# Kernel optimization log

Hardware: AMD Instinct MI355X
Metric: run time of the kernel (lower is better)

## Reference

```python
import jax, jax.numpy as jnp
import numpy as np


def _conv1d(x, w, b):
    # x: (B, Cin, T_padded), w: (Cout, Cin, K), b: (Cout,) -> (B, Cout, T_out)
    y = jax.lax.conv_general_dilated(
        x, w, window_strides=(1,), padding='VALID',
        dimension_numbers=('NCH', 'OIH', 'NCH'))
    return y + b[None, :, None]


def setup_inputs() -> dict:
    key = jax.random.key(0)
    ks = jax.random.split(key, 7)
    B, C, T, H = 32, 64, 8192, 256
    W = 0.05  # small init scale (xavier-ish, keeps exp(log_s) stable)
    return {
        'x': jax.random.normal(ks[0], (B, C, T), dtype=jnp.float32),
        'w_in': jax.random.normal(ks[1], (H, C, 3), dtype=jnp.float32) * W,
        'b_in': jax.random.normal(ks[2], (H,), dtype=jnp.float32) * W,
        'w_mid': jax.random.normal(ks[3], (H, H, 3), dtype=jnp.float32) * W,
        'b_mid': jax.random.normal(ks[4], (H,), dtype=jnp.float32) * W,
        'w_out': jax.random.normal(ks[5], (2 * C, H, 3), dtype=jnp.float32) * W,
        'b_out': jax.random.normal(ks[6], (2 * C,), dtype=jnp.float32) * W,
        'alpha': jnp.ones((1, C, 1), dtype=jnp.float32),
        'beta': jnp.zeros((1, C, 1), dtype=jnp.float32),
    }


def reference(x, w_in, b_in, w_mid, b_mid, w_out, b_out, alpha, beta):
    C = x.shape[1]
    # causal shift: drop last timestep, left-pad 3 -> conv(k=3) yields T outputs
    x_in = jnp.pad(x[:, :, :-1], ((0, 0), (0, 0), (3, 0)))
    rs = _conv1d(x_in, w_in, b_in)                                  # (B, H, T)
    rs = _conv1d(jnp.pad(rs, ((0, 0), (0, 0), (2, 0))), w_mid, b_mid)
    rs = _conv1d(jnp.pad(rs, ((0, 0), (0, 0), (2, 0))), w_out, b_out)  # (B, 2C, T)
    log_s, t = rs[:, :C, :], rs[:, C:, :]
    log_s = alpha * jnp.tanh(log_s) + beta
    z = jnp.exp(log_s) * x + t
    return z
```

## Files before the change

kernel.cpp:

```cpp
#include <hip/hip_runtime.h>
#include <cmath>

typedef __attribute__((ext_vector_type(8))) short short8;
typedef __attribute__((ext_vector_type(4))) float f32x4;

#define B_   32
#define C_   64
#define T_   8192
#define H_   256
#define TT   64

#define XS_ROWB 144
#define RS_ROWB 528
#define RS1_OFF 0
#define RS2_OFF 43296
#define XS_OFF  43296
#define RS3_OFF 0
#define LDS_BYTES 78144

#define A1_SZ 98304
#define A2_SZ 393216
#define A3_SZ 196608
#define AW_TOTAL (A1_SZ + A2_SZ + A3_SZ)

__device__ __forceinline__ unsigned short f2bf(float f) {
    unsigned u = __builtin_bit_cast(unsigned, f);
    u += 0x7fffu + ((u >> 16) & 1u);
    return (unsigned short)(u >> 16);
}

__device__ __forceinline__ unsigned cvtpk(float lo, float hi) {
    unsigned r;
    asm("v_cvt_pk_bf16_f32 %0, %1, %2" : "=v"(r) : "v"(lo), "v"(hi));
    return r;
}

__global__ void pack_w(const float* __restrict__ w1, const float* __restrict__ w2,
                       const float* __restrict__ w3, unsigned short* __restrict__ ws)
{
    int id = blockIdx.x * 256 + threadIdx.x;
    const float* w; int MT, KT, Cin; unsigned short* dst;
    if (id < 6144)       {             w = w1; MT = 16; KT = 2; Cin = 64;  dst = ws; }
    else if (id < 30720) { id -= 6144; w = w2; MT = 16; KT = 8; Cin = 256; dst = ws + A1_SZ/2; }
    else if (id < 43008) { id -= 30720; w = w3; MT = 8; KT = 8; Cin = 256; dst = ws + (A1_SZ+A2_SZ)/2; }
    else return;
    const int lane = id & 63;
    int f = id >> 6;
    const int kt = f % KT; f /= KT;
    const int mt = f % MT;
    const int tap = f / MT;
    const int h  = mt*16 + (lane & 15);
    const int c0 = kt*32 + (lane >> 4)*8;
    unsigned short* o = dst + (size_t)id * 8;
    #pragma unroll
    for (int j = 0; j < 8; ++j)
        o[j] = f2bf(w[((size_t)(h*Cin + c0 + j))*3 + tap]);
}

__device__ __forceinline__ short8 ldA(const char* base, int frag, int lane) {
    return *(const short8*)(base + ((size_t)frag*64 + lane)*16);
}

__global__ __launch_bounds__(512, 4)
void arflow_mfma(const float* __restrict__ x,
                 const float* __restrict__ b_in, const float* __restrict__ b_mid,
                 const float* __restrict__ b_out,
                 const float* __restrict__ alpha, const float* __restrict__ beta,
                 const char* __restrict__ wpk,
                 float* __restrict__ out)
{
    __shared__ __align__(16) char lds[LDS_BYTES];
    unsigned short* xs = (unsigned short*)(lds + XS_OFF);
    char* rs1 = lds + RS1_OFF;
    char* rs2 = lds + RS2_OFF;

    const char* wA1 = wpk;
    const char* wA2 = wpk + A1_SZ;
    const char* wA3 = wpk + A1_SZ + A2_SZ;

    const int b   = blockIdx.y;
    const int t0  = blockIdx.x * TT;
    const int tid = threadIdx.x;
    const int lane = tid & 63;
    const int wid  = tid >> 6;
    const int l15 = lane & 15, l4 = lane >> 4;

    {
        const int rr = tid & 63, cg = tid >> 6;
        #pragma unroll
        for (int p = 0; p < 4; ++p) {
            const int c = cg*8 + p*2;
            const float* xc0 = x + ((size_t)b*C_ + c)*T_;
            const float* xc1 = xc0 + T_;
            {
                const int r = rr; const int t = t0 - 19 + r;
                float v0 = 0.f, v1 = 0.f;
                if (t >= 0) { v0 = xc0[t]; v1 = xc1[t]; }
                *(unsigned*)(&xs[r*72 + c]) = cvtpk(v0, v1);
            }
            {
                const int r = rr + 64;
                if (r < 83) {
                    const int t = t0 - 19 + r;
                    *(unsigned*)(&xs[r*72 + c]) = cvtpk(xc0[t], xc1[t]);
                }
            }
        }
        if (tid < 264) ((unsigned*)rs1)[tid] = 0u;
    }
    __syncthreads();

    {
        const int mt0 = wid*2;
        f32x4 acc[2][5];
        #pragma unroll
        for (int m = 0; m < 2; ++m) {
            const f32x4 bv = *(const f32x4*)(b_in + (mt0+m)*16 + l4*4);
            #pragma unroll
            for (int nt = 0; nt < 5; ++nt) acc[m][nt] = bv;
        }
        int nb[5];
        #pragma unroll
        for (int nt = 0; nt < 5; ++nt)
            nb[nt] = XS_OFF + (16*nt + l15)*XS_ROWB + l4*16;
        short8 Ab[2][2];
        #pragma unroll
        for (int m = 0; m < 2; ++m) Ab[0][m] = ldA(wA1, (mt0+m)*2, lane);
        #pragma unroll
        for (int kt = 0; kt < 6; ++kt) {
            const int cur = kt & 1;
            const int tap = kt >> 1, ck = kt & 1;
            if (kt < 5) {
                const int kn = kt+1, tapn = kn>>1, ckn = kn&1;
                #pragma unroll
                for (int m = 0; m < 2; ++m)
                    Ab[cur^1][m] = ldA(wA1, (tapn*16 + mt0+m)*2 + ckn, lane);
            }
            __builtin_amdgcn_s_setprio(1);
            #pragma unroll
            for (int nt = 0; nt < 5; ++nt) {
                const short8 Bf = *(const short8*)(lds + nb[nt] + tap*XS_ROWB + ck*64);
                #pragma unroll
                for (int m = 0; m < 2; ++m)
                    acc[m][nt] = __builtin_amdgcn_mfma_f32_16x16x32_bf16(Ab[cur][m], Bf, acc[m][nt], 0, 0, 0);
            }
            __builtin_amdgcn_s_setprio(0);
        }
        #pragma unroll
        for (int nt = 0; nt < 5; ++nt) {
            const int tt16 = 16*nt + l15;
            const int t = t0 - 16 + tt16;
            char* dst0 = rs1 + (2 + tt16)*RS_ROWB;
            #pragma unroll
            for (int m = 0; m < 2; ++m) {
                const f32x4 a = acc[m][nt];
                unsigned long long pk = 0ull;
                if (t >= 0)
                    pk = (unsigned long long)cvtpk(a.x, a.y)
                       | ((unsigned long long)cvtpk(a.z, a.w) << 32);
                *(unsigned long long*)(dst0 + ((mt0+m)*16 + l4*4)*2) = pk;
            }
        }
    }
    __syncthreads();

    {
        const int mg = wid >> 1, ng = wid & 1;
        const int ntb = ng ? 3 : 0, ncnt = ng ? 2 : 3;
        f32x4 acc[4][3];
        #pragma unroll
        for (int m = 0; m < 4; ++m) {
            const f32x4 bv = *(const f32x4*)(b_mid + (mg*4+m)*16 + l4*4);
            #pragma unroll
            for (int nt = 0; nt < 3; ++nt) acc[m][nt] = bv;
        }
        int nb[3];
        #pragma unroll
        for (int nt = 0; nt < 3; ++nt)
            nb[nt] = RS1_OFF + (16*(ntb+nt) + l15)*RS_ROWB + l4*16;
        short8 Ab[2][4];
        #pragma unroll
        for (int m = 0; m < 4; ++m) Ab[0][m] = ldA(wA2, (mg*4+m)*8, lane);
        #pragma unroll
        for (int kt = 0; kt < 24; ++kt) {
            const int cur = kt & 1;
            const int tap = kt >> 3, ck = kt & 7;
            if (kt < 23) {
                const int kn = kt+1, tapn = kn>>3, ckn = kn&7;
                #pragma unroll
                for (int m = 0; m < 4; ++m)
                    Ab[cur^1][m] = ldA(wA2, (tapn*16 + mg*4+m)*8 + ckn, lane);
            }
            __builtin_amdgcn_s_setprio(1);
            #pragma unroll
            for (int nt = 0; nt < 3; ++nt) if (nt < ncnt) {
                const short8 Bf = *(const short8*)(lds + nb[nt] + tap*RS_ROWB + ck*64);
                #pragma unroll
                for (int m = 0; m < 4; ++m)
                    acc[m][nt] = __builtin_amdgcn_mfma_f32_16x16x32_bf16(Ab[cur][m], Bf, acc[m][nt], 0, 0, 0);
            }
            __builtin_amdgcn_s_setprio(0);
        }
        #pragma unroll
        for (int nt = 0; nt < 3; ++nt) if (nt < ncnt) {
            const int tt16 = 16*(ntb+nt) + l15;
            const int r2row = tt16 - 14;
            if (r2row >= 0) {
                const int t = t0 - 16 + tt16;
                char* dst0 = rs2 + r2row*RS_ROWB;
                #pragma unroll
                for (int m = 0; m < 4; ++m) {
                    const f32x4 a = acc[m][nt];
                    unsigned long long pk = 0ull;
                    if (t >= 0)
                        pk = (unsigned long long)cvtpk(a.x, a.y)
                           | ((unsigned long long)cvtpk(a.z, a.w) << 32);
                    *(unsigned long long*)(dst0 + ((mg*4+m)*16 + l4*4)*2) = pk;
                }
            }
        }
    }
    __syncthreads();

    float xv[8];
    {
        #pragma unroll
        for (int m = 0; m < 8; ++m) {
            const int e = tid + m*512;
            const int c = e >> 6, tl = e & 63;
            xv[m] = x[((size_t)b*C_ + c)*T_ + t0 + tl];
        }
    }

    {
        const int mt = wid;
        f32x4 acc[4];
        {
            const f32x4 bv = *(const f32x4*)(b_out + mt*16 + l4*4);
            #pragma unroll
            for (int nt = 0; nt < 4; ++nt) acc[nt] = bv;
        }
        int nb[4];
        #pragma unroll
        for (int nt = 0; nt < 4; ++nt)
            nb[nt] = RS2_OFF + (16*nt + l15)*RS_ROWB + l4*16;
        short8 Ab[2];
        Ab[0] = ldA(wA3, mt*8 + 0, lane);
        Ab[1] = ldA(wA3, mt*8 + 1, lane);
        #pragma unroll
        for (int kt = 0; kt < 24; ++kt) {
            const int cur = kt & 1;
            const int tap = kt >> 3, ck = kt & 7;
            __builtin_amdgcn_s_setprio(1);
            #pragma unroll
            for (int nt = 0; nt < 4; ++nt) {
                const short8 Bf = *(const short8*)(lds + nb[nt] + tap*RS_ROWB + ck*64);
                acc[nt] = __builtin_amdgcn_mfma_f32_16x16x32_bf16(Ab[cur], Bf, acc[nt], 0, 0, 0);
            }
            __builtin_amdgcn_s_setprio(0);
            if (kt + 2 < 24) {
                const int kn = kt+2, tapn = kn>>3, ckn = kn&7;
                Ab[cur] = ldA(wA3, (tapn*8 + mt)*8 + ckn, lane);
            }
        }
        #pragma unroll
        for (int nt = 0; nt < 4; ++nt) {
            char* dst0 = lds + RS3_OFF + (16*nt + l15)*RS_ROWB;
            *(f32x4*)(dst0 + (mt*16 + l4*4)*4) = acc[nt];
        }
    }
    __syncthreads();

    {
        const float* rs3f = (const float*)(lds + RS3_OFF);
        #pragma unroll
        for (int m = 0; m < 8; ++m) {
            const int e = tid + m*512;
            const int c = e >> 6, tl = e & 63;
            const float ls = rs3f[tl*132 + c];
            const float tv = rs3f[tl*132 + c + 64];
            const float e2 = __expf(2.f * ls);
            const float th = fmaf(-2.f, __builtin_amdgcn_rcpf(e2 + 1.f), 1.f);
            const float lsv = fmaf(alpha[c], th, beta[c]);
            out[((size_t)b*C_ + c)*T_ + t0 + tl] = fmaf(__expf(lsv), xv[m], tv);
        }
    }
}

extern "C" void kernel_launch(void* const* d_in, const int* in_sizes, int n_in,
                              void* d_out, int out_size, void* d_ws, size_t ws_size,
                              hipStream_t stream) {
    const float* x     = (const float*)d_in[0];
    const float* w_in  = (const float*)d_in[1];
    const float* b_in  = (const float*)d_in[2];
    const float* w_mid = (const float*)d_in[3];
    const float* b_mid = (const float*)d_in[4];
    const float* w_out = (const float*)d_in[5];
    const float* b_out = (const float*)d_in[6];
    const float* alpha = (const float*)d_in[7];
    const float* beta  = (const float*)d_in[8];
    float* out = (float*)d_out;

    if (ws_size < (size_t)AW_TOTAL) return;

    hipLaunchKernelGGL(pack_w, dim3(168), dim3(256), 0, stream,
                       w_in, w_mid, w_out, (unsigned short*)d_ws);
    hipLaunchKernelGGL(arflow_mfma, dim3(T_/TT, B_), dim3(512), 0, stream,
                       x, b_in, b_mid, b_out, alpha, beta, (const char*)d_ws, out);
}
```

Measured before the change: 215.5 us.

## Widen time tile to 96 and reuse one LDS buffer across stages

Raises the per-block time tile from 64 to 96 outputs, which lowers the relative halo recomputation in the three stacked convolutions and reduces the total number of blocks. The last tile overruns T, so loads and stores are now bounds-checked. The intermediate activations now share one LDS buffer, with added barriers so each stage finishes reading before the next overwrites it. The output GEMM work is re-split across waves as 2 M-tiles by 3 N-tiles. LDS grows to about 77KB and there are more accumulators per wave, which may lower occupancy, and the partial last tile wastes some work.

Measured after the change: 450.2 us. +108.9%, slower.

```diff
diff --git a/kernel.cpp b/kernel.cpp
--- a/kernel.cpp
+++ b/kernel.cpp
@@ -8,15 +8,14 @@
 #define C_   64
 #define T_   8192
 #define H_   256
-#define TT   64
-
+#define TT   96
+#define NTB  86
+
+#define RS_ROWB 528
 #define XS_ROWB 144
-#define RS_ROWB 528
-#define RS1_OFF 0
-#define RS2_OFF 43296
-#define XS_OFF  43296
-#define RS3_OFF 0
-#define LDS_BYTES 78144
+#define BUF_OFF 0
+#define XS_OFF  60192
+#define LDS_BYTES (60192 + 115*144)
 
 #define A1_SZ 98304
 #define A2_SZ 393216
@@ -71,8 +70,7 @@
 {
     __shared__ __align__(16) char lds[LDS_BYTES];
     unsigned short* xs = (unsigned short*)(lds + XS_OFF);
-    char* rs1 = lds + RS1_OFF;
-    char* rs2 = lds + RS2_OFF;
+    char* buf = lds + BUF_OFF;
 
     const char* wA1 = wpk;
     const char* wA2 = wpk + A1_SZ;
@@ -93,35 +91,37 @@
             const float* xc0 = x + ((size_t)b*C_ + c)*T_;
             const float* xc1 = xc0 + T_;
             {
-                const int r = rr; const int t = t0 - 19 + r;
+                const int t = t0 - 19 + rr;
                 float v0 = 0.f, v1 = 0.f;
-                if (t >= 0) { v0 = xc0[t]; v1 = xc1[t]; }
-                *(unsigned*)(&xs[r*72 + c]) = cvtpk(v0, v1);
+                if (t >= 0 && t < T_) { v0 = xc0[t]; v1 = xc1[t]; }
+                *(unsigned*)(&xs[rr*72 + c]) = cvtpk(v0, v1);
             }
             {
                 const int r = rr + 64;
-                if (r < 83) {
+                if (r < 115) {
                     const int t = t0 - 19 + r;
-                    *(unsigned*)(&xs[r*72 + c]) = cvtpk(xc0[t], xc1[t]);
+                    float v0 = 0.f, v1 = 0.f;
+                    if (t < T_) { v0 = xc0[t]; v1 = xc1[t]; }
+                    *(unsigned*)(&xs[r*72 + c]) = cvtpk(v0, v1);
                 }
             }
         }
-        if (tid < 264) ((unsigned*)rs1)[tid] = 0u;
+        if (tid < 264) ((unsigned*)buf)[tid] = 0u;
     }
     __syncthreads();
 
     {
         const int mt0 = wid*2;
-        f32x4 acc[2][5];
+        f32x4 acc[2][7];
         #pragma unroll
         for (int m = 0; m < 2; ++m) {
             const f32x4 bv = *(const f32x4*)(b_in + (mt0+m)*16 + l4*4);
             #pragma unroll
-            for (int nt = 0; nt < 5; ++nt) acc[m][nt] = bv;
-        }
-        int nb[5];
-        #pragma unroll
-        for (int nt = 0; nt < 5; ++nt)
+            for (int nt = 0; nt < 7; ++nt) acc[m][nt] = bv;
+        }
+        int nb[7];
+        #pragma unroll
+        for (int nt = 0; nt < 7; ++nt)
             nb[nt] = XS_OFF + (16*nt + l15)*XS_ROWB + l4*16;
         short8 Ab[2][2];
         #pragma unroll
@@ -138,7 +138,7 @@
             }
             __builtin_amdgcn_s_setprio(1);
             #pragma unroll
-            for (int nt = 0; nt < 5; ++nt) {
+            for (int nt = 0; nt < 7; ++nt) {
                 const short8 Bf = *(const short8*)(lds + nb[nt] + tap*XS_ROWB + ck*64);
                 #pragma unroll
                 for (int m = 0; m < 2; ++m)
@@ -147,10 +147,10 @@
             __builtin_amdgcn_s_setprio(0);
         }
         #pragma unroll
-        for (int nt = 0; nt < 5; ++nt) {
+        for (int nt = 0; nt < 7; ++nt) {
             const int tt16 = 16*nt + l15;
             const int t = t0 - 16 + tt16;
-            char* dst0 = rs1 + (2 + tt16)*RS_ROWB;
+            char* dst0 = buf + (2 + tt16)*RS_ROWB;
             #pragma unroll
             for (int m = 0; m < 2; ++m) {
                 const f32x4 a = acc[m][nt];
@@ -166,18 +166,18 @@
 
     {
         const int mg = wid >> 1, ng = wid & 1;
-        const int ntb = ng ? 3 : 0, ncnt = ng ? 2 : 3;
-        f32x4 acc[4][3];
+        const int ntb = ng ? 4 : 0, ncnt = ng ? 3 : 4;
+        f32x4 acc[4][4];
         #pragma unroll
         for (int m = 0; m < 4; ++m) {
             const f32x4 bv = *(const f32x4*)(b_mid + (mg*4+m)*16 + l4*4);
             #pragma unroll
-            for (int nt = 0; nt < 3; ++nt) acc[m][nt] = bv;
-        }
-        int nb[3];
-        #pragma unroll
-        for (int nt = 0; nt < 3; ++nt)
-            nb[nt] = RS1_OFF + (16*(ntb+nt) + l15)*RS_ROWB + l4*16;
+            for (int nt = 0; nt < 4; ++nt) acc[m][nt] = bv;
+        }
+        int nb[4];
+        #pragma unroll
+        for (int nt = 0; nt < 4; ++nt)
+            nb[nt] = BUF_OFF + (16*(ntb+nt) + l15)*RS_ROWB + l4*16;
         short8 Ab[2][4];
         #pragma unroll
         for (int m = 0; m < 4; ++m) Ab[0][m] = ldA(wA2, (mg*4+m)*8, lane);
@@ -193,7 +193,7 @@
             }
             __builtin_amdgcn_s_setprio(1);
             #pragma unroll
-            for (int nt = 0; nt < 3; ++nt) if (nt < ncnt) {
+            for (int nt = 0; nt < 4; ++nt) if (nt < ncnt) {
                 const short8 Bf = *(const short8*)(lds + nb[nt] + tap*RS_ROWB + ck*64);
                 #pragma unroll
                 for (int m = 0; m < 4; ++m)
@@ -201,13 +201,14 @@
             }
             __builtin_amdgcn_s_setprio(0);
         }
-        #pragma unroll
-        for (int nt = 0; nt < 3; ++nt) if (nt < ncnt) {
+        __syncthreads();
+        #pragma unroll
+        for (int nt = 0; nt < 4; ++nt) if (nt < ncnt) {
             const int tt16 = 16*(ntb+nt) + l15;
             const int r2row = tt16 - 14;
             if (r2row >= 0) {
                 const int t = t0 - 16 + tt16;
-                char* dst0 = rs2 + r2row*RS_ROWB;
+                char* dst0 = buf + r2row*RS_ROWB;
                 #pragma unroll
                 for (int m = 0; m < 4; ++m) {
                     const f32x4 a = acc[m][nt];
@@ -220,69 +221,87 @@
             }
         }
     }
+
+    float xv[12];
+    {
+        #pragma unroll
+        for (int m = 0; m < 12; ++m) {
+            const int g = tid + m*512;
+            const int c = (int)((unsigned)g / 96u);
+            const int tl = g - c*96;
+            const int t = t0 + tl;
+            xv[m] = (t < T_) ? x[((size_t)b*C_ + c)*T_ + t] : 0.f;
+        }
+    }
     __syncthreads();
 
-    float xv[8];
-    {
-        #pragma unroll
-        for (int m = 0; m < 8; ++m) {
-            const int e = tid + m*512;
-            const int c = e >> 6, tl = e & 63;
-            xv[m] = x[((size_t)b*C_ + c)*T_ + t0 + tl];
-        }
-    }
-
-    {
-        const int mt = wid;
-        f32x4 acc[4];
-        {
-            const f32x4 bv = *(const f32x4*)(b_out + mt*16 + l4*4);
-            #pragma unroll
-            for (int nt = 0; nt < 4; ++nt) acc[nt] = bv;
-        }
-        int nb[4];
-        #pragma unroll
-        for (int nt = 0; nt < 4; ++nt)
-            nb[nt] = RS2_OFF + (16*nt + l15)*RS_ROWB + l4*16;
-        short8 Ab[2];
-        Ab[0] = ldA(wA3, mt*8 + 0, lane);
-        Ab[1] = ldA(wA3, mt*8 + 1, lane);
+    {
+        const int mg = wid >> 1;
+        const int ng = wid & 1;
+        const int ntb = ng * 3;
+        f32x4 acc[2][3];
+        #pragma unroll
+        for (int m = 0; m < 2; ++m) {
+            const f32x4 bv = *(const f32x4*)(b_out + (mg*2+m)*16 + l4*4);
+            #pragma unroll
+            for (int nt = 0; nt < 3; ++nt) acc[m][nt] = bv;
+        }
+        int nb[3];
+        #pragma unroll
+        for (int nt = 0; nt < 3; ++nt)
+            nb[nt] = BUF_OFF + (16*(ntb+nt) + l15)*RS_ROWB + l4*16;
+        short8 Ab[2][2];
+        #pragma unroll
+        for (int m = 0; m < 2; ++m) {
+            Ab[0][m] = ldA(wA3, ((mg*2+m))*8 + 0, lane);
+            Ab[1][m] = ldA(wA3, ((mg*2+m))*8 + 1, lane);
+        }
         #pragma unroll
         for (int kt = 0; kt < 24; ++kt) {
             const int cur = kt & 1;
             const int tap = kt >> 3, ck = kt & 7;
             __builtin_amdgcn_s_setprio(1);
             #pragma unroll
-            for (int nt = 0; nt < 4; ++nt) {
+            for (int nt = 0; nt < 3; ++nt) {
                 const short8 Bf = *(const short8*)(lds + nb[nt] + tap*RS_ROWB + ck*64);
-                acc[nt] = __builtin_amdgcn_mfma_f32_16x16x32_bf16(Ab[cur], Bf, acc[nt], 0, 0, 0);
+                #pragma unroll
+                for (int m = 0; m < 2; ++m)
+                    acc[m][nt] = __builtin_amdgcn_mfma_f32_16x16x32_bf16(Ab[cur][m], Bf, acc[m][nt], 0, 0, 0);
             }
             __builtin_amdgcn_s_setprio(0);
             if (kt + 2 < 24) {
                 const int kn = kt+2, tapn = kn>>3, ckn = kn&7;
-                Ab[cur] = ldA(wA3, (tapn*8 + mt)*8 + ckn, lane);
-            }
-        }
-        #pragma unroll
-        for (int nt = 0; nt < 4; ++nt) {
-            char* dst0 = lds + RS3_OFF + (16*nt + l15)*RS_ROWB;
-            *(f32x4*)(dst0 + (mt*16 + l4*4)*4) = acc[nt];
+                #pragma unroll
+                for (int m = 0; m < 2; ++m)
+                    Ab[cur][m] = ldA(wA3, (tapn*8 + mg*2+m)*8 + ckn, lane);
+            }
+        }
+        __syncthreads();
+        #pragma unroll
+        for (int nt = 0; nt < 3; ++nt) {
+            char* dst0 = buf + (16*(ntb+nt) + l15)*RS_ROWB;
+            #pragma unroll
+            for (int m = 0; m < 2; ++m)
+                *(f32x4*)(dst0 + ((mg*2+m)*16 + l4*4)*4) = acc[m][nt];
         }
     }
     __syncthreads();
 
     {
-        const float* rs3f = (const float*)(lds + RS3_OFF);
-        #pragma unroll
-        for (int m = 0; m < 8; ++m) {
-            const int e = tid + m*512;
-            const int c = e >> 6, tl = e & 63;
+        const float* rs3f = (const float*)buf;
+        #pragma unroll
+        for (int m = 0; m < 12; ++m) {
+            const int g = tid + m*512;
+            const int c = (int)((unsigned)g / 96u);
+            const int tl = g - c*96;
+            const int t = t0 + tl;
             const float ls = rs3f[tl*132 + c];
             const float tv = rs3f[tl*132 + c + 64];
             const float e2 = __expf(2.f * ls);
             const float th = fmaf(-2.f, __builtin_amdgcn_rcpf(e2 + 1.f), 1.f);
             const float lsv = fmaf(alpha[c], th, beta[c]);
-            out[((size_t)b*C_ + c)*T_ + t0 + tl] = fmaf(__expf(lsv), xv[m], tv);
+            if (t < T_)
+                out[((size_t)b*C_ + c)*T_ + t] = fmaf(__expf(lsv), xv[m], tv);
         }
     }
 }
@@ -305,6 +324,6 @@
 
     hipLaunchKernelGGL(pack_w, dim3(168), dim3(256), 0, stream,
                        w_in, w_mid, w_out, (unsigned short*)d_ws);
-    hipLaunchKernelGGL(arflow_mfma, dim3(T_/TT, B_), dim3(512), 0, stream,
+    hipLaunchKernelGGL(arflow_mfma, dim3(NTB, B_), dim3(512), 0, stream,
                        x, b_in, b_mid, b_out, alpha, beta, (const char*)d_ws, out);
 }
```

## Double the time tile and switch to 32x32x16 MFMA with in-place LDS reuse

Applied to the files above, without the earlier changes.

Raises the per-block time tile from 64 to 128 steps. This halves the fraction of halo recomputation: each block recomputes 16 extra rows for conv1 and 2 for conv2. All three conv GEMMs switch from 16x16x32 to 32x32x16 bf16 MFMA with a matching repacked weight layout, and the intermediate activations share one LDS buffer overwritten in place, with an extra barrier. Occupancy drops to 2 blocks per CU because of the larger LDS footprint and accumulators, and the halved grid may reduce latency hiding.

Measured after the change: 234.1 us. 1.09x slower.

```diff
diff --git a/kernel.cpp b/kernel.cpp
--- a/kernel.cpp
+++ b/kernel.cpp
@@ -1,26 +1,25 @@
 #include <hip/hip_runtime.h>
 #include <cmath>
 
-typedef __attribute__((ext_vector_type(8))) short short8;
-typedef __attribute__((ext_vector_type(4))) float f32x4;
+typedef __attribute__((ext_vector_type(8)))  short short8;
+typedef __attribute__((ext_vector_type(4)))  float f32x4;
+typedef __attribute__((ext_vector_type(16))) float f32x16;
 
 #define B_   32
 #define C_   64
 #define T_   8192
 #define H_   256
-#define TT   64
-
+#define TT   128
+
+#define RS_ROWB 528
 #define XS_ROWB 144
-#define RS_ROWB 528
-#define RS1_OFF 0
-#define RS2_OFF 43296
-#define XS_OFF  43296
-#define RS3_OFF 0
-#define LDS_BYTES 78144
-
-#define A1_SZ 98304
-#define A2_SZ 393216
-#define A3_SZ 196608
+#define BUF_OFF 0
+#define XS_OFF  77088
+#define LDS_BYTES (77088 + 162*144)
+
+#define A1_SZ  98304
+#define A2_SZ  393216
+#define A3_SZ  196608
 #define AW_TOTAL (A1_SZ + A2_SZ + A3_SZ)
 
 __device__ __forceinline__ unsigned short f2bf(float f) {
@@ -28,7 +27,6 @@
     u += 0x7fffu + ((u >> 16) & 1u);
     return (unsigned short)(u >> 16);
 }
-
 __device__ __forceinline__ unsigned cvtpk(float lo, float hi) {
     unsigned r;
     asm("v_cvt_pk_bf16_f32 %0, %1, %2" : "=v"(r) : "v"(lo), "v"(hi));
@@ -40,17 +38,17 @@
 {
     int id = blockIdx.x * 256 + threadIdx.x;
     const float* w; int MT, KT, Cin; unsigned short* dst;
-    if (id < 6144)       {             w = w1; MT = 16; KT = 2; Cin = 64;  dst = ws; }
-    else if (id < 30720) { id -= 6144; w = w2; MT = 16; KT = 8; Cin = 256; dst = ws + A1_SZ/2; }
-    else if (id < 43008) { id -= 30720; w = w3; MT = 8; KT = 8; Cin = 256; dst = ws + (A1_SZ+A2_SZ)/2; }
+    if (id < 6144)       {             w = w1; MT = 8; KT = 4;  Cin = 64;  dst = ws; }
+    else if (id < 30720) { id -= 6144; w = w2; MT = 8; KT = 16; Cin = 256; dst = ws + A1_SZ/2; }
+    else if (id < 43008) { id -= 30720; w = w3; MT = 4; KT = 16; Cin = 256; dst = ws + (A1_SZ+A2_SZ)/2; }
     else return;
     const int lane = id & 63;
     int f = id >> 6;
     const int kt = f % KT; f /= KT;
     const int mt = f % MT;
     const int tap = f / MT;
-    const int h  = mt*16 + (lane & 15);
-    const int c0 = kt*32 + (lane >> 4)*8;
+    const int h  = mt*32 + (lane & 31);
+    const int c0 = kt*16 + (lane >> 5)*8;
     unsigned short* o = dst + (size_t)id * 8;
     #pragma unroll
     for (int j = 0; j < 8; ++j)
@@ -61,7 +59,7 @@
     return *(const short8*)(base + ((size_t)frag*64 + lane)*16);
 }
 
-__global__ __launch_bounds__(512, 4)
+__global__ __launch_bounds__(512, 2)
 void arflow_mfma(const float* __restrict__ x,
                  const float* __restrict__ b_in, const float* __restrict__ b_mid,
                  const float* __restrict__ b_out,
@@ -71,8 +69,7 @@
 {
     __shared__ __align__(16) char lds[LDS_BYTES];
     unsigned short* xs = (unsigned short*)(lds + XS_OFF);
-    char* rs1 = lds + RS1_OFF;
-    char* rs2 = lds + RS2_OFF;
+    char* buf = lds + BUF_OFF;
 
     const char* wA1 = wpk;
     const char* wA2 = wpk + A1_SZ;
@@ -83,200 +80,220 @@
     const int tid = threadIdx.x;
     const int lane = tid & 63;
     const int wid  = tid >> 6;
-    const int l15 = lane & 15, l4 = lane >> 4;
-
-    {
-        const int rr = tid & 63, cg = tid >> 6;
-        #pragma unroll
-        for (int p = 0; p < 4; ++p) {
-            const int c = cg*8 + p*2;
+    const int l31 = lane & 31, l5 = lane >> 5;
+
+    {
+        const int rr = tid & 127, cg = tid >> 7;
+        const int t = t0 - 19 + rr;
+        #pragma unroll
+        for (int p = 0; p < 8; ++p) {
+            const int c = cg*16 + p*2;
             const float* xc0 = x + ((size_t)b*C_ + c)*T_;
             const float* xc1 = xc0 + T_;
-            {
-                const int r = rr; const int t = t0 - 19 + r;
-                float v0 = 0.f, v1 = 0.f;
-                if (t >= 0) { v0 = xc0[t]; v1 = xc1[t]; }
-                *(unsigned*)(&xs[r*72 + c]) = cvtpk(v0, v1);
-            }
-            {
-                const int r = rr + 64;
-                if (r < 83) {
-                    const int t = t0 - 19 + r;
-                    *(unsigned*)(&xs[r*72 + c]) = cvtpk(xc0[t], xc1[t]);
-                }
-            }
-        }
-        if (tid < 264) ((unsigned*)rs1)[tid] = 0u;
+            float v0 = 0.f, v1 = 0.f;
+            if (t >= 0) { v0 = xc0[t]; v1 = xc1[t]; }
+            *(unsigned*)(&xs[rr*72 + c]) = cvtpk(v0, v1);
+            if (rr < 19) {
+                const int t2 = t + 128;
+                *(unsigned*)(&xs[(rr+128)*72 + c]) = cvtpk(xc0[t2], xc1[t2]);
+            }
+        }
     }
     __syncthreads();
 
     {
-        const int mt0 = wid*2;
-        f32x4 acc[2][5];
-        #pragma unroll
-        for (int m = 0; m < 2; ++m) {
-            const f32x4 bv = *(const f32x4*)(b_in + (mt0+m)*16 + l4*4);
-            #pragma unroll
-            for (int nt = 0; nt < 5; ++nt) acc[m][nt] = bv;
-        }
+        const int mt = wid;
+        f32x4 bq[4];
+        #pragma unroll
+        for (int q = 0; q < 4; ++q)
+            bq[q] = *(const f32x4*)(b_in + mt*32 + q*8 + l5*4);
+        f32x16 acc[5];
+        #pragma unroll
+        for (int nt = 0; nt < 5; ++nt)
+            #pragma unroll
+            for (int q = 0; q < 4; ++q) {
+                acc[nt][4*q+0] = bq[q][0]; acc[nt][4*q+1] = bq[q][1];
+                acc[nt][4*q+2] = bq[q][2]; acc[nt][4*q+3] = bq[q][3];
+            }
         int nb[5];
         #pragma unroll
         for (int nt = 0; nt < 5; ++nt)
-            nb[nt] = XS_OFF + (16*nt + l15)*XS_ROWB + l4*16;
-        short8 Ab[2][2];
-        #pragma unroll
-        for (int m = 0; m < 2; ++m) Ab[0][m] = ldA(wA1, (mt0+m)*2, lane);
-        #pragma unroll
-        for (int kt = 0; kt < 6; ++kt) {
+            nb[nt] = XS_OFF + (32*nt + l31)*XS_ROWB + l5*16;
+        short8 Ab[2];
+        Ab[0] = ldA(wA1, mt*4, lane);
+        #pragma unroll
+        for (int kt = 0; kt < 12; ++kt) {
             const int cur = kt & 1;
-            const int tap = kt >> 1, ck = kt & 1;
-            if (kt < 5) {
-                const int kn = kt+1, tapn = kn>>1, ckn = kn&1;
-                #pragma unroll
-                for (int m = 0; m < 2; ++m)
-                    Ab[cur^1][m] = ldA(wA1, (tapn*16 + mt0+m)*2 + ckn, lane);
+            const int tap = kt >> 2, ck = kt & 3;
+            if (kt < 11) {
+                const int kn = kt + 1;
+                Ab[cur^1] = ldA(wA1, ((kn>>2)*8 + mt)*4 + (kn&3), lane);
             }
             __builtin_amdgcn_s_setprio(1);
             #pragma unroll
             for (int nt = 0; nt < 5; ++nt) {
-                const short8 Bf = *(const short8*)(lds + nb[nt] + tap*XS_ROWB + ck*64);
-                #pragma unroll
-                for (int m = 0; m < 2; ++m)
-                    acc[m][nt] = __builtin_amdgcn_mfma_f32_16x16x32_bf16(Ab[cur][m], Bf, acc[m][nt], 0, 0, 0);
+                const short8 Bf = *(const short8*)(lds + nb[nt] + tap*XS_ROWB + ck*32);
+                acc[nt] = __builtin_amdgcn_mfma_f32_32x32x16_bf16(Ab[cur], Bf, acc[nt], 0, 0, 0);
             }
             __builtin_amdgcn_s_setprio(0);
         }
         #pragma unroll
         for (int nt = 0; nt < 5; ++nt) {
-            const int tt16 = 16*nt + l15;
-            const int t = t0 - 16 + tt16;
-            char* dst0 = rs1 + (2 + tt16)*RS_ROWB;
-            #pragma unroll
-            for (int m = 0; m < 2; ++m) {
-                const f32x4 a = acc[m][nt];
-                unsigned long long pk = 0ull;
-                if (t >= 0)
-                    pk = (unsigned long long)cvtpk(a.x, a.y)
-                       | ((unsigned long long)cvtpk(a.z, a.w) << 32);
-                *(unsigned long long*)(dst0 + ((mt0+m)*16 + l4*4)*2) = pk;
-            }
-        }
-    }
-    __syncthreads();
-
-    {
-        const int mg = wid >> 1, ng = wid & 1;
-        const int ntb = ng ? 3 : 0, ncnt = ng ? 2 : 3;
-        f32x4 acc[4][3];
-        #pragma unroll
-        for (int m = 0; m < 4; ++m) {
-            const f32x4 bv = *(const f32x4*)(b_mid + (mg*4+m)*16 + l4*4);
-            #pragma unroll
-            for (int nt = 0; nt < 3; ++nt) acc[m][nt] = bv;
-        }
-        int nb[3];
-        #pragma unroll
-        for (int nt = 0; nt < 3; ++nt)
-            nb[nt] = RS1_OFF + (16*(ntb+nt) + l15)*RS_ROWB + l4*16;
-        short8 Ab[2][4];
-        #pragma unroll
-        for (int m = 0; m < 4; ++m) Ab[0][m] = ldA(wA2, (mg*4+m)*8, lane);
-        #pragma unroll
-        for (int kt = 0; kt < 24; ++kt) {
-            const int cur = kt & 1;
-            const int tap = kt >> 3, ck = kt & 7;
-            if (kt < 23) {
-                const int kn = kt+1, tapn = kn>>3, ckn = kn&7;
-                #pragma unroll
-                for (int m = 0; m < 4; ++m)
-                    Ab[cur^1][m] = ldA(wA2, (tapn*16 + mg*4+m)*8 + ckn, lane);
-            }
-            __builtin_amdgcn_s_setprio(1);
-            #pragma unroll
-            for (int nt = 0; nt < 3; ++nt) if (nt < ncnt) {
-                const short8 Bf = *(const short8*)(lds + nb[nt] + tap*RS_ROWB + ck*64);
-                #pragma unroll
-                for (int m = 0; m < 4; ++m)
-                    acc[m][nt] = __builtin_amdgcn_mfma_f32_16x16x32_bf16(Ab[cur][m], Bf, acc[m][nt], 0, 0, 0);
-            }
-            __builtin_amdgcn_s_setprio(0);
-        }
-        #pragma unroll
-        for (int nt = 0; nt < 3; ++nt) if (nt < ncnt) {
-            const int tt16 = 16*(ntb+nt) + l15;
-            const int r2row = tt16 - 14;
-            if (r2row >= 0) {
-                const int t = t0 - 16 + tt16;
-                char* dst0 = rs2 + r2row*RS_ROWB;
-                #pragma unroll
-                for (int m = 0; m < 4; ++m) {
-                    const f32x4 a = acc[m][nt];
+            const int rb = 2 + 32*nt + l31;
+            const int t  = t0 - 16 + 32*nt + l31;
+            if (rb <= 145) {
+                char* dst0 = buf + rb*RS_ROWB + mt*64;
+                #pragma unroll
+                for (int q = 0; q < 4; ++q) {
                     unsigned long long pk = 0ull;
                     if (t >= 0)
-                        pk = (unsigned long long)cvtpk(a.x, a.y)
-                           | ((unsigned long long)cvtpk(a.z, a.w) << 32);
-                    *(unsigned long long*)(dst0 + ((mg*4+m)*16 + l4*4)*2) = pk;
+                        pk = (unsigned long long)cvtpk(acc[nt][4*q+0], acc[nt][4*q+1])
+                           | ((unsigned long long)cvtpk(acc[nt][4*q+2], acc[nt][4*q+3]) << 32);
+                    *(unsigned long long*)(dst0 + q*16 + l5*8) = pk;
                 }
             }
         }
     }
     __syncthreads();
 
-    float xv[8];
-    {
-        #pragma unroll
-        for (int m = 0; m < 8; ++m) {
+    {
+        const int mg = wid >> 1, ng = wid & 1;
+        const int mt0 = mg*2;
+        const int ntb = ng ? 3 : 0, ncnt = ng ? 2 : 3;
+        f32x16 acc[2][3];
+        #pragma unroll
+        for (int m = 0; m < 2; ++m) {
+            f32x4 bq[4];
+            #pragma unroll
+            for (int q = 0; q < 4; ++q)
+                bq[q] = *(const f32x4*)(b_mid + (mt0+m)*32 + q*8 + l5*4);
+            #pragma unroll
+            for (int nt = 0; nt < 3; ++nt)
+                #pragma unroll
+                for (int q = 0; q < 4; ++q) {
+                    acc[m][nt][4*q+0] = bq[q][0]; acc[m][nt][4*q+1] = bq[q][1];
+                    acc[m][nt][4*q+2] = bq[q][2]; acc[m][nt][4*q+3] = bq[q][3];
+                }
+        }
+        int nb[3];
+        #pragma unroll
+        for (int nt = 0; nt < 3; ++nt)
+            nb[nt] = BUF_OFF + (14 + 32*(ntb+nt) + l31)*RS_ROWB + l5*16;
+        short8 Ab[2][2];
+        #pragma unroll
+        for (int m = 0; m < 2; ++m) Ab[0][m] = ldA(wA2, (mt0+m)*16, lane);
+        #pragma unroll
+        for (int kt = 0; kt < 48; ++kt) {
+            const int cur = kt & 1;
+            const int tap = kt >> 4, ck = kt & 15;
+            if (kt < 47) {
+                const int kn = kt + 1, tapn = kn >> 4, ckn = kn & 15;
+                #pragma unroll
+                for (int m = 0; m < 2; ++m)
+                    Ab[cur^1][m] = ldA(wA2, (tapn*8 + mt0+m)*16 + ckn, lane);
+            }
+            __builtin_amdgcn_s_setprio(1);
+            #pragma unroll
+            for (int nt = 0; nt < 3; ++nt) if (nt < ncnt) {
+                const short8 Bf = *(const short8*)(lds + nb[nt] + tap*RS_ROWB + ck*32);
+                #pragma unroll
+                for (int m = 0; m < 2; ++m)
+                    acc[m][nt] = __builtin_amdgcn_mfma_f32_32x32x16_bf16(Ab[cur][m], Bf, acc[m][nt], 0, 0, 0);
+            }
+            __builtin_amdgcn_s_setprio(0);
+        }
+        __syncthreads();
+        #pragma unroll
+        for (int nt = 0; nt < 3; ++nt) if (nt < ncnt) {
+            const int r2 = 32*(ntb+nt) + l31;
+            const int t  = t0 - 2 + r2;
+            if (r2 <= 129) {
+                #pragma unroll
+                for (int m = 0; m < 2; ++m) {
+                    char* dst0 = buf + r2*RS_ROWB + (mt0+m)*64;
+                    #pragma unroll
+                    for (int q = 0; q < 4; ++q) {
+                        unsigned long long pk = 0ull;
+                        if (t >= 0)
+                            pk = (unsigned long long)cvtpk(acc[m][nt][4*q+0], acc[m][nt][4*q+1])
+                               | ((unsigned long long)cvtpk(acc[m][nt][4*q+2], acc[m][nt][4*q+3]) << 32);
+                        *(unsigned long long*)(dst0 + q*16 + l5*8) = pk;
+                    }
+                }
+            }
+        }
+    }
+
+    float xv[16];
+    #pragma unroll
+    for (int m = 0; m < 16; ++m) {
+        const int e = tid + m*512;
+        const int c = e >> 7, tl = e & 127;
+        xv[m] = x[((size_t)b*C_ + c)*T_ + t0 + tl];
+    }
+    __syncthreads();
+
+    {
+        const int mt = wid & 3, ng = wid >> 2;
+        const int ntb = ng*2;
+        f32x4 bq[4];
+        #pragma unroll
+        for (int q = 0; q < 4; ++q)
+            bq[q] = *(const f32x4*)(b_out + mt*32 + q*8 + l5*4);
+        f32x16 acc[2];
+        #pragma unroll
+        for (int nt = 0; nt < 2; ++nt)
+            #pragma unroll
+            for (int q = 0; q < 4; ++q) {
+                acc[nt][4*q+0] = bq[q][0]; acc[nt][4*q+1] = bq[q][1];
+                acc[nt][4*q+2] = bq[q][2]; acc[nt][4*q+3] = bq[q][3];
+            }
+        int nb[2];
+        #pragma unroll
+        for (int nt = 0; nt < 2; ++nt)
+            nb[nt] = BUF_OFF + (32*(ntb+nt) + l31)*RS_ROWB + l5*16;
+        short8 Ab[4];
+        Ab[0] = ldA(wA3, mt*16 + 0, lane);
+        Ab[1] = ldA(wA3, mt*16 + 1, lane);
+        Ab[2] = ldA(wA3, mt*16 + 2, lane);
+        #pragma unroll
+        for (int kt = 0; kt < 48; ++kt) {
+            const int cur = kt & 3;
+            const int tap = kt >> 4, ck = kt & 15;
+            if (kt < 45) {
+                const int kn = kt + 3;
+                Ab[(kt+3)&3] = ldA(wA3, ((kn>>4)*4 + mt)*16 + (kn&15), lane);
+            }
+            __builtin_amdgcn_s_setprio(1);
+            #pragma unroll
+            for (int nt = 0; nt < 2; ++nt) {
+                const short8 Bf = *(const short8*)(lds + nb[nt] + tap*RS_ROWB + ck*32);
+                acc[nt] = __builtin_amdgcn_mfma_f32_32x32x16_bf16(Ab[cur], Bf, acc[nt], 0, 0, 0);
+            }
+            __builtin_amdgcn_s_setprio(0);
+        }
+        __syncthreads();
+        #pragma unroll
+        for (int nt = 0; nt < 2; ++nt) {
+            const int row = 32*(ntb+nt) + l31;
+            char* dst0 = buf + row*RS_ROWB + mt*128;
+            #pragma unroll
+            for (int q = 0; q < 4; ++q) {
+                f32x4 v;
+                v[0] = acc[nt][4*q+0]; v[1] = acc[nt][4*q+1];
+                v[2] = acc[nt][4*q+2]; v[3] = acc[nt][4*q+3];
+                *(f32x4*)(dst0 + q*32 + l5*16) = v;
+            }
+        }
+    }
+    __syncthreads();
+
+    {
+        const float* rs3f = (const float*)buf;
+        #pragma unroll
+        for (int m = 0; m < 16; ++m) {
             const int e = tid + m*512;
-            const int c = e >> 6, tl = e & 63;
-            xv[m] = x[((size_t)b*C_ + c)*T_ + t0 + tl];
-        }
-    }
-
-    {
-        const int mt = wid;
-        f32x4 acc[4];
-        {
-            const f32x4 bv = *(const f32x4*)(b_out + mt*16 + l4*4);
-            #pragma unroll
-            for (int nt = 0; nt < 4; ++nt) acc[nt] = bv;
-        }
-        int nb[4];
-        #pragma unroll
-        for (int nt = 0; nt < 4; ++nt)
-            nb[nt] = RS2_OFF + (16*nt + l15)*RS_ROWB + l4*16;
-        short8 Ab[2];
-        Ab[0] = ldA(wA3, mt*8 + 0, lane);
-        Ab[1] = ldA(wA3, mt*8 + 1, lane);
-        #pragma unroll
-        for (int kt = 0; kt < 24; ++kt) {
-            const int cur = kt & 1;
-            const int tap = kt >> 3, ck = kt & 7;
-            __builtin_amdgcn_s_setprio(1);
-            #pragma unroll
-            for (int nt = 0; nt < 4; ++nt) {
-                const short8 Bf = *(const short8*)(lds + nb[nt] + tap*RS_ROWB + ck*64);
-                acc[nt] = __builtin_amdgcn_mfma_f32_16x16x32_bf16(Ab[cur], Bf, acc[nt], 0, 0, 0);
-            }
-            __builtin_amdgcn_s_setprio(0);
-            if (kt + 2 < 24) {
-                const int kn = kt+2, tapn = kn>>3, ckn = kn&7;
-                Ab[cur] = ldA(wA3, (tapn*8 + mt)*8 + ckn, lane);
-            }
-        }
-        #pragma unroll
-        for (int nt = 0; nt < 4; ++nt) {
-            char* dst0 = lds + RS3_OFF + (16*nt + l15)*RS_ROWB;
-            *(f32x4*)(dst0 + (mt*16 + l4*4)*4) = acc[nt];
-        }
-    }
-    __syncthreads();
-
-    {
-        const float* rs3f = (const float*)(lds + RS3_OFF);
-        #pragma unroll
-        for (int m = 0; m < 8; ++m) {
-            const int e = tid + m*512;
-            const int c = e >> 6, tl = e & 63;
+            const int c = e >> 7, tl = e & 127;
             const float ls = rs3f[tl*132 + c];
             const float tv = rs3f[tl*132 + c + 64];
             const float e2 = __expf(2.f * ls);
```
